# Kernel tuning notes

Measured on AMD Instinct MI355X. Metric: run time of the kernel, lower is better.

Reference implementation:

```python
import jax, jax.numpy as jnp
import numpy as np

B, T, D, H, DK, DV = 4, 2048, 1024, 16, 64, 64


def setup_inputs() -> dict:
    key = jax.random.key(0)
    ks = jax.random.split(key, 7)
    # Glorot-uniform-ish init for weights
    def glorot(k, shape, fan_in, fan_out):
        lim = jnp.sqrt(6.0 / (fan_in + fan_out))
        return jax.random.uniform(k, shape, jnp.float32, -lim, lim)
    Q = jax.random.normal(ks[0], (B, T, D), jnp.float32)
    K = jax.random.normal(ks[1], (B, T, D), jnp.float32)
    V = jax.random.normal(ks[2], (B, T, D), jnp.float32)
    WQ = glorot(ks[3], (H, D, DK), D, DK)
    WK = glorot(ks[4], (H, D, DK), D, DK)
    WV = glorot(ks[5], (H, D, DV), D, DV)
    WO = glorot(ks[6], (H * DV, D), H * DV, D)
    # additive causal mask: 1 where attention is blocked (j > i)
    mask = jnp.triu(jnp.ones((T, T), jnp.float32), k=1)[None, None]  # [1,1,T,T]
    return {"Q": Q, "K": K, "V": V, "WQ": WQ, "WK": WK, "WV": WV, "WO": WO, "mask": mask}


def reference(Q, K, V, WQ, WK, WV, WO, mask):
    Qh = jnp.einsum('btd,hdk->bhtk', Q, WQ)
    Kh = jnp.einsum('btd,hdk->bhtk', K, WK)
    Vh = jnp.einsum('btd,hdv->bhtv', V, WV)
    dk = jnp.asarray(Qh.shape[-1], Qh.dtype)
    logits = jnp.einsum('bhtk,bhsk->bhts', Qh, Kh) / jnp.sqrt(dk)
    logits = logits + mask * (-1e9)
    attn = jax.nn.softmax(logits, axis=-1)
    Ah = jnp.einsum('bhts,bhsv->bhtv', attn, Vh)          # [B,H,T,DV]
    A = jnp.transpose(Ah, (0, 2, 1, 3)).reshape(Ah.shape[0], Ah.shape[2], -1)  # [B,T,H*DV]
    return A @ WO
```

## Files before the change

### kernel.cpp

```cpp
#include <hip/hip_runtime.h>
#include <hip/hip_bf16.h>

#define B_ 4
#define T_ 2048
#define D_ 1024
#define H_ 16

typedef __attribute__((ext_vector_type(8))) short bf16x8;
typedef __attribute__((ext_vector_type(4))) float f32x4;
typedef __attribute__((ext_vector_type(4))) unsigned short u16x4;

__device__ __forceinline__ unsigned short f2bf(float x) {
  union { float f; unsigned u; } v; v.f = x;
  unsigned r = v.u + 0x7fffu + ((v.u >> 16) & 1u);
  return (unsigned short)(r >> 16);
}

__device__ __forceinline__ unsigned pack_bf2(float a, float b) {
  __hip_bfloat162 h = __float22bfloat162_rn(float2{a, b});
  union { __hip_bfloat162 h; unsigned u; } cv; cv.h = h; return cv.u;
}

__device__ __forceinline__ void gload_lds16(const void* g, void* l) {
  __builtin_amdgcn_global_load_lds(
      (const __attribute__((address_space(1))) unsigned int*)g,
      (__attribute__((address_space(3))) unsigned int*)l, 16, 0, 0);
}

#define MFMA16(a, b, c) __builtin_amdgcn_mfma_f32_16x16x32_bf16((a), (b), (c), 0, 0, 0)

__global__ __launch_bounds__(256) void conv3(
    const float4* __restrict__ Q, const float4* __restrict__ K,
    const float4* __restrict__ V, u16x4* __restrict__ Qb,
    u16x4* __restrict__ Kb, u16x4* __restrict__ Vb) {
  const int seg = blockIdx.x >> 10;
  const int sb  = blockIdx.x & 1023;
  const float4* s = (seg == 0) ? Q : (seg == 1) ? K : V;
  u16x4* d       = (seg == 0) ? Qb : (seg == 1) ? Kb : Vb;
  int i = sb * 256 + threadIdx.x;
#pragma unroll
  for (int it = 0; it < 8; ++it, i += 262144) {
    float4 v = s[i];
    u16x4 o;
    o[0] = f2bf(v.x); o[1] = f2bf(v.y); o[2] = f2bf(v.z); o[3] = f2bf(v.w);
    d[i] = o;
  }
}

__global__ __launch_bounds__(256) void trans4(
    const float* __restrict__ WQ, const float* __restrict__ WK,
    const float* __restrict__ WV, const float* __restrict__ WO,
    unsigned short* __restrict__ WqT, unsigned short* __restrict__ WkT,
    unsigned short* __restrict__ WvT, unsigned short* __restrict__ WOt) {
  __shared__ float tile[64][65];
  const int seg = blockIdx.x >> 8;
  const int sub = blockIdx.x & 255;
  const float* src = (seg == 0) ? WQ : (seg == 1) ? WK : (seg == 2) ? WV : WO;
  unsigned short* dst = (seg == 0) ? WqT : (seg == 1) ? WkT : (seg == 2) ? WvT : WOt;
  const int DK = (seg == 3) ? 1024 : 64;
  int h, dt, ktile;
  if (seg == 3) { h = 0; dt = sub >> 4; ktile = sub & 15; }
  else          { h = sub >> 4; dt = sub & 15; ktile = 0; }
  const int d0 = dt * 64, k0 = ktile * 64;
  const int tx = threadIdx.x & 63, ty = threadIdx.x >> 6;
  const float* s = src + (size_t)h * 1024 * DK;
#pragma unroll
  for (int i = 0; i < 16; ++i) {
    int row = i * 4 + ty;
    tile[row][tx] = s[(size_t)(d0 + row) * DK + k0 + tx];
  }
  __syncthreads();
  unsigned short* dd = dst + (size_t)h * DK * 1024;
#pragma unroll
  for (int i = 0; i < 16; ++i) {
    int kk = i * 4 + ty;
    dd[(size_t)(k0 + kk) * 1024 + d0 + tx] = f2bf(tile[tx][kk]);
  }
}

__device__ __forceinline__ void gemm_body(
    const unsigned short* __restrict__ A, const unsigned short* __restrict__ Bt,
    void* __restrict__ C, int bid, int nTilesN, int mode, float scale) {
  __shared__ unsigned short As[128 * 64];
  __shared__ unsigned short Bs[128 * 64];
  const int bm = bid / nTilesN, bn = bid % nTilesN;
  const int m0 = bm * 128, n0 = bn * 128;
  const int tid = threadIdx.x;
  const int wave = tid >> 6, lane = tid & 63;
  const int wr = wave >> 1, wc = wave & 1;

  f32x4 acc[4][4];
#pragma unroll
  for (int m = 0; m < 4; ++m)
#pragma unroll
    for (int n = 0; n < 4; ++n) acc[m][n] = 0.f;

  const int soff = wave * 1024 + lane * 16;
  const char* Afr = (const char*)As + (wr * 64 + (lane & 15)) * 128 + (lane >> 4) * 16;
  const char* Bfr = (const char*)Bs + (wc * 64 + (lane & 15)) * 128 + (lane >> 4) * 16;

  for (int kt = 0; kt < 16; ++kt) {
    __syncthreads();
#pragma unroll
    for (int i = 0; i < 4; ++i) {
      int o2 = i * 4096 + soff;
      int row = o2 >> 7, colb = o2 & 127;
      gload_lds16((const char*)(A + (size_t)(m0 + row) * 1024 + kt * 64) + colb,
                  (char*)As + i * 4096 + wave * 1024);
      gload_lds16((const char*)(Bt + (size_t)(n0 + row) * 1024 + kt * 64) + colb,
                  (char*)Bs + i * 4096 + wave * 1024);
    }
    __syncthreads();
#pragma unroll
    for (int kk = 0; kk < 2; ++kk) {
      bf16x8 af[4], bf[4];
#pragma unroll
      for (int m = 0; m < 4; ++m) af[m] = *(const bf16x8*)(Afr + m * 2048 + kk * 64);
#pragma unroll
      for (int n = 0; n < 4; ++n) bf[n] = *(const bf16x8*)(Bfr + n * 2048 + kk * 64);
#pragma unroll
      for (int m = 0; m < 4; ++m)
#pragma unroll
        for (int n = 0; n < 4; ++n) acc[m][n] = MFMA16(af[m], bf[n], acc[m][n]);
    }
  }

  const int rbase = m0 + wr * 64 + ((lane >> 4) << 2);
  const int cbase = n0 + wc * 64 + (lane & 15);
#pragma unroll
  for (int m = 0; m < 4; ++m)
#pragma unroll
    for (int n = 0; n < 4; ++n)
#pragma unroll
      for (int r = 0; r < 4; ++r) {
        int row = rbase + m * 16 + r;
        int col = cbase + n * 16;
        float v = acc[m][n][r] * scale;
        if (mode == 0) {
          ((float*)C)[(size_t)row * 1024 + col] = v;
        } else if (mode == 1) {
          int b = row >> 11, t = row & 2047, h = col >> 6, k = col & 63;
          ((unsigned short*)C)[(((size_t)(b * H_ + h) * T_) + t) * 64 + k] = f2bf(v);
        } else {
          int h = row >> 6, vv = row & 63, b = col >> 11, t = col & 2047;
          ((unsigned short*)C)[(((size_t)(b * H_ + h) * 64) + vv) * T_ + t] = f2bf(v);
        }
      }
}

__global__ __launch_bounds__(256) void gemm_proj3(
    const unsigned short* __restrict__ Qbf, const unsigned short* __restrict__ WqT,
    unsigned short* __restrict__ Qh,
    const unsigned short* __restrict__ Kbf, const unsigned short* __restrict__ WkT,
    unsigned short* __restrict__ Kh,
    const unsigned short* __restrict__ WvT, const unsigned short* __restrict__ Vbf,
    unsigned short* __restrict__ VhT, float qscale) {
  const int bid = blockIdx.x;
  const int wid = (bid & 7) * 192 + (bid >> 3);
  const int seg = wid / 512, sub = wid % 512;
  const unsigned short* A  = (seg == 0) ? Qbf : (seg == 1) ? Kbf : WvT;
  const unsigned short* Bt = (seg == 0) ? WqT : (seg == 1) ? WkT : Vbf;
  void* C = (seg == 0) ? (void*)Qh : (seg == 1) ? (void*)Kh : (void*)VhT;
  gemm_body(A, Bt, C, sub, (seg == 2) ? 64 : 8, (seg == 2) ? 2 : 1,
            (seg == 0) ? qscale : 1.0f);
}

__global__ __launch_bounds__(256) void gemm_out(
    const unsigned short* __restrict__ A, const unsigned short* __restrict__ Bt,
    float* __restrict__ C) {
  const int bid = blockIdx.x;
  const int wid = (bid & 7) * 64 + (bid >> 3);
  gemm_body(A, Bt, C, wid, 8, 0, 1.0f);
}

__global__ __launch_bounds__(256) void attn_fwd(
    const unsigned short* __restrict__ Qh, const unsigned short* __restrict__ Kh,
    const unsigned short* __restrict__ VhT, unsigned short* __restrict__ Abuf) {
  __shared__ unsigned short Ks[2][64 * 64];
  __shared__ unsigned short Vs[2][64 * 64];
  __shared__ unsigned short Ps[4][16 * 64];

  const int bid = blockIdx.x;
  const int wid = ((bid & 7) << 7) | (bid >> 3);
  const int p  = wid & 15;
  const int bh = wid >> 4;
  const int b = bh >> 4, h = bh & 15;
  const int tid = threadIdx.x;
  const int wave = tid >> 6, lane = tid & 63;
  const int lq = lane & 15;
  const int hi = lane >> 4;
  const int nkt = 32 - p;

  int q0[2];
  q0[0] = (31 - p) * 64 + wave * 16;
  q0[1] = p * 64 + wave * 16;

  const char* Kbase = (const char*)(Kh + (size_t)bh * T_ * 64);
  const char* Vbase = (const char*)(VhT + (size_t)bh * 64 * T_);

  int srow[2], scol[2], sdst[2];
#pragma unroll
  for (int i = 0; i < 2; ++i) {
    int o = i * 4096 + wave * 1024 + lane * 16;
    srow[i] = o >> 7;
    scol[i] = (o & 127) ^ ((srow[i] & 7) << 4);
    sdst[i] = i * 4096 + wave * 1024;
  }

  bf16x8 qf[2][2];
#pragma unroll
  for (int j = 0; j < 2; ++j) {
    const unsigned short* qp = Qh + ((size_t)bh * T_ + q0[j] + lq) * 64 + hi * 8;
    qf[j][0] = *(const bf16x8*)qp;
    qf[j][1] = *(const bf16x8*)(qp + 32);
  }

  f32x4 o[2][4];
#pragma unroll
  for (int j = 0; j < 2; ++j)
#pragma unroll
    for (int n = 0; n < 4; ++n) o[j][n] = 0.f;
  float m_run[2] = {-1e30f, -1e30f}, l_run[2] = {0.f, 0.f};

  const int pswz = (lq & 7) << 4;
  char* pw = (char*)&Ps[wave][0] + lq * 128;

  auto stage = [&](int buf, int kt) {
#pragma unroll
    for (int i = 0; i < 2; ++i) {
      gload_lds16(Kbase + (size_t)(kt * 64 + srow[i]) * 128 + scol[i],
                  (char*)Ks[buf] + sdst[i]);
      gload_lds16(Vbase + (size_t)srow[i] * (T_ * 2) + kt * 128 + scol[i],
                  (char*)Vs[buf] + sdst[i]);
    }
  };

  stage(0, 0);
  asm volatile("s_waitcnt vmcnt(0)" ::: "memory");
  __builtin_amdgcn_s_barrier();

  int cur = 0;
  for (int kt = 0; kt < nkt; ++kt) {
    const int s0 = kt * 64;
    if (kt + 1 < nkt) stage(cur ^ 1, kt + 1);

    const char* KsB = (const char*)Ks[cur];
    const char* VsB = (const char*)Vs[cur];

#pragma unroll
    for (int j = 0; j < 2; ++j) {
      if (j == 1 && kt > p) continue;

      f32x4 sc[4];
      __builtin_amdgcn_s_setprio(1);
#pragma unroll
      for (int c = 0; c < 4; ++c) {
        int r = c * 16 + lq;
        const char* kb = KsB + r * 128;
        int sw = (r & 7) << 4;
        bf16x8 ka0 = *(const bf16x8*)(kb + ((hi * 16) ^ sw));
        bf16x8 ka1 = *(const bf16x8*)(kb + ((64 + hi * 16) ^ sw));
        f32x4 z = 0.f;
        z = MFMA16(ka0, qf[j][0], z);
        sc[c] = MFMA16(ka1, qf[j][1], z);
      }
      __builtin_amdgcn_s_setprio(0);

      if (s0 + 63 > q0[j]) {
        int qg = q0[j] + lq;
#pragma unroll
        for (int c = 0; c < 4; ++c)
#pragma unroll
          for (int r = 0; r < 4; ++r) {
            int sg = s0 + c * 16 + hi * 4 + r;
            if (sg > qg) sc[c][r] = -1e30f;
          }
      }

      float pmax = sc[0][0];
#pragma unroll
      for (int c = 0; c < 4; ++c)
#pragma unroll
        for (int r = 0; r < 4; ++r) pmax = fmaxf(pmax, sc[c][r]);
      pmax = fmaxf(pmax, __shfl_xor(pmax, 16));
      pmax = fmaxf(pmax, __shfl_xor(pmax, 32));

      if (!__all(pmax - m_run[j] <= 8.f)) {
        float mnew = fmaxf(m_run[j], pmax);
        float corr = __builtin_amdgcn_exp2f(m_run[j] - mnew);
        float cr[4];
#pragma unroll
        for (int r = 0; r < 4; ++r) cr[r] = __shfl(corr, hi * 4 + r);
#pragma unroll
        for (int n = 0; n < 4; ++n)
#pragma unroll
          for (int r = 0; r < 4; ++r) o[j][n][r] *= cr[r];
        l_run[j] *= corr;
        m_run[j] = mnew;
      }

      float psum = 0.f;
#pragma unroll
      for (int c = 0; c < 4; ++c)
#pragma unroll
        for (int r = 0; r < 4; ++r) {
          float pv = __builtin_amdgcn_exp2f(sc[c][r] - m_run[j]);
          sc[c][r] = pv;
          psum += pv;
        }
      psum += __shfl_xor(psum, 16);
      psum += __shfl_xor(psum, 32);
      l_run[j] += psum;

#pragma unroll
      for (int c = 0; c < 4; ++c) {
        uint2 pk;
        pk.x = pack_bf2(sc[c][0], sc[c][1]);
        pk.y = pack_bf2(sc[c][2], sc[c][3]);
        *(uint2*)(pw + ((c * 32 + hi * 8) ^ pswz)) = pk;
      }

      __builtin_amdgcn_s_setprio(1);
#pragma unroll
      for (int ks = 0; ks < 2; ++ks) {
        bf16x8 pa = *(const bf16x8*)(pw + ((ks * 64 + hi * 16) ^ pswz));
#pragma unroll
        for (int n = 0; n < 4; ++n) {
          int rv = n * 16 + lq;
          bf16x8 vb = *(const bf16x8*)(VsB + rv * 128 +
                                       ((ks * 64 + hi * 16) ^ ((rv & 7) << 4)));
          o[j][n] = MFMA16(pa, vb, o[j][n]);
        }
      }
      __builtin_amdgcn_s_setprio(0);
    }

    asm volatile("s_waitcnt vmcnt(0)" ::: "memory");
    __builtin_amdgcn_s_barrier();
    cur ^= 1;
  }

#pragma unroll
  for (int j = 0; j < 2; ++j) {
    float inv[4];
#pragma unroll
    for (int r = 0; r < 4; ++r)
      inv[r] = 1.0f / __shfl(l_run[j], hi * 4 + r);
#pragma unroll
    for (int r = 0; r < 4; ++r) {
      int t = q0[j] + hi * 4 + r;
      size_t base = ((size_t)b * T_ + t) * 1024 + h * 64 + lq;
#pragma unroll
      for (int n = 0; n < 4; ++n)
        Abuf[base + n * 16] = f2bf(o[j][n][r] * inv[r]);
    }
  }
}

extern "C" void kernel_launch(void* const* d_in, const int* in_sizes, int n_in,
                              void* d_out, int out_size, void* d_ws, size_t ws_size,
                              hipStream_t stream) {
  (void)in_sizes; (void)n_in; (void)out_size; (void)ws_size;
  const float* Q  = (const float*)d_in[0];
  const float* K  = (const float*)d_in[1];
  const float* V  = (const float*)d_in[2];
  const float* WQ = (const float*)d_in[3];
  const float* WK = (const float*)d_in[4];
  const float* WV = (const float*)d_in[5];
  const float* WO = (const float*)d_in[6];
  float* out = (float*)d_out;
  char* ws = (char*)d_ws;

  const size_t SZ_ACT = (size_t)8192 * 1024 * 2;
  const size_t SZ_W   = (size_t)1024 * 1024 * 2;
  unsigned short* Qbf = (unsigned short*)(ws);
  unsigned short* Kbf = (unsigned short*)(ws + SZ_ACT);
  unsigned short* Vbf = (unsigned short*)(ws + 2 * SZ_ACT);
  unsigned short* WqT = (unsigned short*)(ws + 3 * SZ_ACT);
  unsigned short* WkT = (unsigned short*)(ws + 3 * SZ_ACT + SZ_W);
  unsigned short* WvT = (unsigned short*)(ws + 3 * SZ_ACT + 2 * SZ_W);
  unsigned short* WOt = (unsigned short*)(ws + 3 * SZ_ACT + 3 * SZ_W);
  unsigned short* Qh  = (unsigned short*)(ws + 3 * SZ_ACT + 4 * SZ_W);
  unsigned short* Kh  = (unsigned short*)(ws + 4 * SZ_ACT + 4 * SZ_W);
  unsigned short* VhT = (unsigned short*)(ws + 5 * SZ_ACT + 4 * SZ_W);
  unsigned short* Abuf = Qbf;

  conv3<<<3072, 256, 0, stream>>>((const float4*)Q, (const float4*)K,
                                  (const float4*)V, (u16x4*)Qbf, (u16x4*)Kbf,
                                  (u16x4*)Vbf);

  trans4<<<1024, 256, 0, stream>>>(WQ, WK, WV, WO, WqT, WkT, WvT, WOt);

  const float qscale = 1.4426950408889634f / 8.0f;
  gemm_proj3<<<1536, 256, 0, stream>>>(Qbf, WqT, Qh, Kbf, WkT, Kh,
                                       WvT, Vbf, VhT, qscale);

  attn_fwd<<<1024, 256, 0, stream>>>(Qh, Kh, VhT, Abuf);

  gemm_out<<<512, 256, 0, stream>>>(Abuf, WOt, out);
}
```

Baseline: 230.4 us.

## Fuse fp32-to-bf16 conversion into projection GEMM loads and keep P in registers

Drops the separate conversion kernel. The projection GEMM now reads fp32 Q/K/V directly, converts to bf16 in registers and stores to LDS, which avoids writing and re-reading bf16 activation copies. In attention, the probability tile no longer round-trips through LDS: it is rearranged into the MFMA A-operand layout with permlane swap instructions, and an occupancy hint is added to launch bounds. The tradeoff is that the GEMM loses the async global-to-LDS path for fp32 operands, so loads go through registers and fetch twice the bytes per tile.

New measurement: 227.1 us, median of 2. No clear change (-1.4%).

```diff
diff --git a/kernel.cpp b/kernel.cpp
--- a/kernel.cpp
+++ b/kernel.cpp
@@ -9,6 +9,7 @@
 typedef __attribute__((ext_vector_type(8))) short bf16x8;
 typedef __attribute__((ext_vector_type(4))) float f32x4;
 typedef __attribute__((ext_vector_type(4))) unsigned short u16x4;
+typedef __attribute__((ext_vector_type(4))) unsigned int u32x4;
 
 __device__ __forceinline__ unsigned short f2bf(float x) {
   union { float f; unsigned u; } v; v.f = x;
@@ -28,24 +29,6 @@
 }
 
 #define MFMA16(a, b, c) __builtin_amdgcn_mfma_f32_16x16x32_bf16((a), (b), (c), 0, 0, 0)
-
-__global__ __launch_bounds__(256) void conv3(
-    const float4* __restrict__ Q, const float4* __restrict__ K,
-    const float4* __restrict__ V, u16x4* __restrict__ Qb,
-    u16x4* __restrict__ Kb, u16x4* __restrict__ Vb) {
-  const int seg = blockIdx.x >> 10;
-  const int sb  = blockIdx.x & 1023;
-  const float4* s = (seg == 0) ? Q : (seg == 1) ? K : V;
-  u16x4* d       = (seg == 0) ? Qb : (seg == 1) ? Kb : Vb;
-  int i = sb * 256 + threadIdx.x;
-#pragma unroll
-  for (int it = 0; it < 8; ++it, i += 262144) {
-    float4 v = s[i];
-    u16x4 o;
-    o[0] = f2bf(v.x); o[1] = f2bf(v.y); o[2] = f2bf(v.z); o[3] = f2bf(v.w);
-    d[i] = o;
-  }
-}
 
 __global__ __launch_bounds__(256) void trans4(
     const float* __restrict__ WQ, const float* __restrict__ WK,
@@ -78,9 +61,10 @@
   }
 }
 
+template <bool AF32, bool BF32, int CMODE>
 __device__ __forceinline__ void gemm_body(
-    const unsigned short* __restrict__ A, const unsigned short* __restrict__ Bt,
-    void* __restrict__ C, int bid, int nTilesN, int mode, float scale) {
+    const void* __restrict__ Ap, const void* __restrict__ Btp,
+    void* __restrict__ C, int bid, int nTilesN, float scale) {
   __shared__ unsigned short As[128 * 64];
   __shared__ unsigned short Bs[128 * 64];
   const int bm = bid / nTilesN, bn = bid % nTilesN;
@@ -105,10 +89,32 @@
     for (int i = 0; i < 4; ++i) {
       int o2 = i * 4096 + soff;
       int row = o2 >> 7, colb = o2 & 127;
-      gload_lds16((const char*)(A + (size_t)(m0 + row) * 1024 + kt * 64) + colb,
-                  (char*)As + i * 4096 + wave * 1024);
-      gload_lds16((const char*)(Bt + (size_t)(n0 + row) * 1024 + kt * 64) + colb,
-                  (char*)Bs + i * 4096 + wave * 1024);
+      if constexpr (AF32) {
+        const float* src = (const float*)Ap + (size_t)(m0 + row) * 1024 + kt * 64 + (colb >> 1);
+        float4 f0 = *(const float4*)src;
+        float4 f1 = *(const float4*)(src + 4);
+        u32x4 w;
+        w[0] = pack_bf2(f0.x, f0.y); w[1] = pack_bf2(f0.z, f0.w);
+        w[2] = pack_bf2(f1.x, f1.y); w[3] = pack_bf2(f1.z, f1.w);
+        *(u32x4*)((char*)As + o2) = w;
+      } else {
+        gload_lds16((const char*)((const unsigned short*)Ap +
+                        (size_t)(m0 + row) * 1024 + kt * 64) + colb,
+                    (char*)As + i * 4096 + wave * 1024);
+      }
+      if constexpr (BF32) {
+        const float* src = (const float*)Btp + (size_t)(n0 + row) * 1024 + kt * 64 + (colb >> 1);
+        float4 f0 = *(const float4*)src;
+        float4 f1 = *(const float4*)(src + 4);
+        u32x4 w;
+        w[0] = pack_bf2(f0.x, f0.y); w[1] = pack_bf2(f0.z, f0.w);
+        w[2] = pack_bf2(f1.x, f1.y); w[3] = pack_bf2(f1.z, f1.w);
+        *(u32x4*)((char*)Bs + o2) = w;
+      } else {
+        gload_lds16((const char*)((const unsigned short*)Btp +
+                        (size_t)(n0 + row) * 1024 + kt * 64) + colb,
+                    (char*)Bs + i * 4096 + wave * 1024);
+      }
     }
     __syncthreads();
 #pragma unroll
@@ -136,9 +142,9 @@
         int row = rbase + m * 16 + r;
         int col = cbase + n * 16;
         float v = acc[m][n][r] * scale;
-        if (mode == 0) {
+        if constexpr (CMODE == 0) {
           ((float*)C)[(size_t)row * 1024 + col] = v;
-        } else if (mode == 1) {
+        } else if constexpr (CMODE == 1) {
           int b = row >> 11, t = row & 2047, h = col >> 6, k = col & 63;
           ((unsigned short*)C)[(((size_t)(b * H_ + h) * T_) + t) * 64 + k] = f2bf(v);
         } else {
@@ -149,20 +155,18 @@
 }
 
 __global__ __launch_bounds__(256) void gemm_proj3(
-    const unsigned short* __restrict__ Qbf, const unsigned short* __restrict__ WqT,
+    const float* __restrict__ Q, const unsigned short* __restrict__ WqT,
     unsigned short* __restrict__ Qh,
-    const unsigned short* __restrict__ Kbf, const unsigned short* __restrict__ WkT,
+    const float* __restrict__ K, const unsigned short* __restrict__ WkT,
     unsigned short* __restrict__ Kh,
-    const unsigned short* __restrict__ WvT, const unsigned short* __restrict__ Vbf,
+    const unsigned short* __restrict__ WvT, const float* __restrict__ V,
     unsigned short* __restrict__ VhT, float qscale) {
   const int bid = blockIdx.x;
   const int wid = (bid & 7) * 192 + (bid >> 3);
   const int seg = wid / 512, sub = wid % 512;
-  const unsigned short* A  = (seg == 0) ? Qbf : (seg == 1) ? Kbf : WvT;
-  const unsigned short* Bt = (seg == 0) ? WqT : (seg == 1) ? WkT : Vbf;
-  void* C = (seg == 0) ? (void*)Qh : (seg == 1) ? (void*)Kh : (void*)VhT;
-  gemm_body(A, Bt, C, sub, (seg == 2) ? 64 : 8, (seg == 2) ? 2 : 1,
-            (seg == 0) ? qscale : 1.0f);
+  if (seg == 0)      gemm_body<true,  false, 1>(Q,   WqT, Qh,  sub, 8,  qscale);
+  else if (seg == 1) gemm_body<true,  false, 1>(K,   WkT, Kh,  sub, 8,  1.0f);
+  else               gemm_body<false, true,  2>(WvT, V,   VhT, sub, 64, 1.0f);
 }
 
 __global__ __launch_bounds__(256) void gemm_out(
@@ -170,15 +174,14 @@
     float* __restrict__ C) {
   const int bid = blockIdx.x;
   const int wid = (bid & 7) * 64 + (bid >> 3);
-  gemm_body(A, Bt, C, wid, 8, 0, 1.0f);
-}
-
-__global__ __launch_bounds__(256) void attn_fwd(
+  gemm_body<false, false, 0>(A, Bt, C, wid, 8, 1.0f);
+}
+
+__global__ __launch_bounds__(256, 5) void attn_fwd(
     const unsigned short* __restrict__ Qh, const unsigned short* __restrict__ Kh,
     const unsigned short* __restrict__ VhT, unsigned short* __restrict__ Abuf) {
   __shared__ unsigned short Ks[2][64 * 64];
   __shared__ unsigned short Vs[2][64 * 64];
-  __shared__ unsigned short Ps[4][16 * 64];
 
   const int bid = blockIdx.x;
   const int wid = ((bid & 7) << 7) | (bid >> 3);
@@ -222,9 +225,6 @@
     for (int n = 0; n < 4; ++n) o[j][n] = 0.f;
   float m_run[2] = {-1e30f, -1e30f}, l_run[2] = {0.f, 0.f};
 
-  const int pswz = (lq & 7) << 4;
-  char* pw = (char*)&Ps[wave][0] + lq * 128;
-
   auto stage = [&](int buf, int kt) {
 #pragma unroll
     for (int i = 0; i < 2; ++i) {
@@ -312,18 +312,25 @@
       psum += __shfl_xor(psum, 32);
       l_run[j] += psum;
 
+      unsigned pk[4][2];
 #pragma unroll
       for (int c = 0; c < 4; ++c) {
-        uint2 pk;
-        pk.x = pack_bf2(sc[c][0], sc[c][1]);
-        pk.y = pack_bf2(sc[c][2], sc[c][3]);
-        *(uint2*)(pw + ((c * 32 + hi * 8) ^ pswz)) = pk;
+        pk[c][0] = pack_bf2(sc[c][0], sc[c][1]);
+        pk[c][1] = pack_bf2(sc[c][2], sc[c][3]);
       }
 
       __builtin_amdgcn_s_setprio(1);
 #pragma unroll
       for (int ks = 0; ks < 2; ++ks) {
-        bf16x8 pa = *(const bf16x8*)(pw + ((ks * 64 + hi * 16) ^ pswz));
+        unsigned a0 = pk[2 * ks][0], b0 = pk[2 * ks + 1][0];
+        unsigned a1 = pk[2 * ks][1], b1 = pk[2 * ks + 1][1];
+        asm("v_permlane32_swap_b32 %0, %1" : "+v"(a0), "+v"(b0));
+        asm("v_permlane16_swap_b32 %0, %1" : "+v"(a0), "+v"(b0));
+        asm("v_permlane32_swap_b32 %0, %1" : "+v"(a1), "+v"(b1));
+        asm("v_permlane16_swap_b32 %0, %1" : "+v"(a1), "+v"(b1));
+        u32x4 pau;
+        pau[0] = a0; pau[1] = a1; pau[2] = b0; pau[3] = b1;
+        bf16x8 pa = __builtin_bit_cast(bf16x8, pau);
 #pragma unroll
         for (int n = 0; n < 4; ++n) {
           int rv = n * 16 + lq;
@@ -373,27 +380,20 @@
 
   const size_t SZ_ACT = (size_t)8192 * 1024 * 2;
   const size_t SZ_W   = (size_t)1024 * 1024 * 2;
-  unsigned short* Qbf = (unsigned short*)(ws);
-  unsigned short* Kbf = (unsigned short*)(ws + SZ_ACT);
-  unsigned short* Vbf = (unsigned short*)(ws + 2 * SZ_ACT);
-  unsigned short* WqT = (unsigned short*)(ws + 3 * SZ_ACT);
-  unsigned short* WkT = (unsigned short*)(ws + 3 * SZ_ACT + SZ_W);
-  unsigned short* WvT = (unsigned short*)(ws + 3 * SZ_ACT + 2 * SZ_W);
-  unsigned short* WOt = (unsigned short*)(ws + 3 * SZ_ACT + 3 * SZ_W);
-  unsigned short* Qh  = (unsigned short*)(ws + 3 * SZ_ACT + 4 * SZ_W);
-  unsigned short* Kh  = (unsigned short*)(ws + 4 * SZ_ACT + 4 * SZ_W);
-  unsigned short* VhT = (unsigned short*)(ws + 5 * SZ_ACT + 4 * SZ_W);
-  unsigned short* Abuf = Qbf;
-
-  conv3<<<3072, 256, 0, stream>>>((const float4*)Q, (const float4*)K,
-                                  (const float4*)V, (u16x4*)Qbf, (u16x4*)Kbf,
-                                  (u16x4*)Vbf);
+  unsigned short* WqT = (unsigned short*)(ws);
+  unsigned short* WkT = (unsigned short*)(ws + SZ_W);
+  unsigned short* WvT = (unsigned short*)(ws + 2 * SZ_W);
+  unsigned short* WOt = (unsigned short*)(ws + 3 * SZ_W);
+  unsigned short* Qh  = (unsigned short*)(ws + 4 * SZ_W);
+  unsigned short* Kh  = (unsigned short*)(ws + 4 * SZ_W + SZ_ACT);
+  unsigned short* VhT = (unsigned short*)(ws + 4 * SZ_W + 2 * SZ_ACT);
+  unsigned short* Abuf = (unsigned short*)(ws + 4 * SZ_W + 3 * SZ_ACT);
 
   trans4<<<1024, 256, 0, stream>>>(WQ, WK, WV, WO, WqT, WkT, WvT, WOt);
 
   const float qscale = 1.4426950408889634f / 8.0f;
-  gemm_proj3<<<1536, 256, 0, stream>>>(Qbf, WqT, Qh, Kbf, WkT, Kh,
-                                       WvT, Vbf, VhT, qscale);
+  gemm_proj3<<<1536, 256, 0, stream>>>(Q, WqT, Qh, K, WkT, Kh,
+                                       WvT, V, VhT, qscale);
 
   attn_fwd<<<1024, 256, 0, stream>>>(Qh, Kh, VhT, Abuf);
 
```

## Merge prep kernels, template GEMM epilogue, use permlane swaps for P operand

Applied to the files above, without the earlier changes.

Merges the input cast and weight transpose kernels into one launch. The GEMM epilogue mode becomes a template parameter so the store branch is resolved at compile time. In attention, the probability tile is rearranged into the MFMA A-operand layout with v_permlane32/16 swaps in registers instead of a round trip through LDS, which removes the Ps buffer and adds a launch_bounds occupancy hint of 5. The permlane lane mapping must match the old LDS swizzle exactly, or the results will be wrong.

New measurement: 221.5 us. -3.9%, faster.

```diff
diff --git a/kernel.cpp b/kernel.cpp
--- a/kernel.cpp
+++ b/kernel.cpp
@@ -9,6 +9,7 @@
 typedef __attribute__((ext_vector_type(8))) short bf16x8;
 typedef __attribute__((ext_vector_type(4))) float f32x4;
 typedef __attribute__((ext_vector_type(4))) unsigned short u16x4;
+typedef __attribute__((ext_vector_type(4))) unsigned int u32x4;
 
 __device__ __forceinline__ unsigned short f2bf(float x) {
   union { float f; unsigned u; } v; v.f = x;
@@ -29,60 +30,62 @@
 
 #define MFMA16(a, b, c) __builtin_amdgcn_mfma_f32_16x16x32_bf16((a), (b), (c), 0, 0, 0)
 
-__global__ __launch_bounds__(256) void conv3(
+__global__ __launch_bounds__(256) void prep(
     const float4* __restrict__ Q, const float4* __restrict__ K,
     const float4* __restrict__ V, u16x4* __restrict__ Qb,
-    u16x4* __restrict__ Kb, u16x4* __restrict__ Vb) {
-  const int seg = blockIdx.x >> 10;
-  const int sb  = blockIdx.x & 1023;
-  const float4* s = (seg == 0) ? Q : (seg == 1) ? K : V;
-  u16x4* d       = (seg == 0) ? Qb : (seg == 1) ? Kb : Vb;
-  int i = sb * 256 + threadIdx.x;
-#pragma unroll
-  for (int it = 0; it < 8; ++it, i += 262144) {
-    float4 v = s[i];
-    u16x4 o;
-    o[0] = f2bf(v.x); o[1] = f2bf(v.y); o[2] = f2bf(v.z); o[3] = f2bf(v.w);
-    d[i] = o;
-  }
-}
-
-__global__ __launch_bounds__(256) void trans4(
+    u16x4* __restrict__ Kb, u16x4* __restrict__ Vb,
     const float* __restrict__ WQ, const float* __restrict__ WK,
     const float* __restrict__ WV, const float* __restrict__ WO,
     unsigned short* __restrict__ WqT, unsigned short* __restrict__ WkT,
     unsigned short* __restrict__ WvT, unsigned short* __restrict__ WOt) {
   __shared__ float tile[64][65];
-  const int seg = blockIdx.x >> 8;
-  const int sub = blockIdx.x & 255;
-  const float* src = (seg == 0) ? WQ : (seg == 1) ? WK : (seg == 2) ? WV : WO;
-  unsigned short* dst = (seg == 0) ? WqT : (seg == 1) ? WkT : (seg == 2) ? WvT : WOt;
-  const int DK = (seg == 3) ? 1024 : 64;
-  int h, dt, ktile;
-  if (seg == 3) { h = 0; dt = sub >> 4; ktile = sub & 15; }
-  else          { h = sub >> 4; dt = sub & 15; ktile = 0; }
-  const int d0 = dt * 64, k0 = ktile * 64;
-  const int tx = threadIdx.x & 63, ty = threadIdx.x >> 6;
-  const float* s = src + (size_t)h * 1024 * DK;
-#pragma unroll
-  for (int i = 0; i < 16; ++i) {
-    int row = i * 4 + ty;
-    tile[row][tx] = s[(size_t)(d0 + row) * DK + k0 + tx];
-  }
-  __syncthreads();
-  unsigned short* dd = dst + (size_t)h * DK * 1024;
-#pragma unroll
-  for (int i = 0; i < 16; ++i) {
-    int kk = i * 4 + ty;
-    dd[(size_t)(k0 + kk) * 1024 + d0 + tx] = f2bf(tile[tx][kk]);
-  }
-}
-
+  const int bidx = blockIdx.x;
+  if (bidx < 3072) {
+    const int seg = bidx >> 10;
+    const int sb  = bidx & 1023;
+    const float4* s = (seg == 0) ? Q : (seg == 1) ? K : V;
+    u16x4* d       = (seg == 0) ? Qb : (seg == 1) ? Kb : Vb;
+    int i = sb * 256 + threadIdx.x;
+#pragma unroll
+    for (int it = 0; it < 8; ++it, i += 262144) {
+      float4 v = s[i];
+      u16x4 o;
+      o[0] = f2bf(v.x); o[1] = f2bf(v.y); o[2] = f2bf(v.z); o[3] = f2bf(v.w);
+      d[i] = o;
+    }
+  } else {
+    const int sub4 = bidx - 3072;
+    const int seg = sub4 >> 8;
+    const int sub = sub4 & 255;
+    const float* src = (seg == 0) ? WQ : (seg == 1) ? WK : (seg == 2) ? WV : WO;
+    unsigned short* dst = (seg == 0) ? WqT : (seg == 1) ? WkT : (seg == 2) ? WvT : WOt;
+    const int DK = (seg == 3) ? 1024 : 64;
+    int h, dt, ktile;
+    if (seg == 3) { h = 0; dt = sub >> 4; ktile = sub & 15; }
+    else          { h = sub >> 4; dt = sub & 15; ktile = 0; }
+    const int d0 = dt * 64, k0 = ktile * 64;
+    const int tx = threadIdx.x & 63, ty = threadIdx.x >> 6;
+    const float* s = src + (size_t)h * 1024 * DK;
+#pragma unroll
+    for (int i = 0; i < 16; ++i) {
+      int row = i * 4 + ty;
+      tile[row][tx] = s[(size_t)(d0 + row) * DK + k0 + tx];
+    }
+    __syncthreads();
+    unsigned short* dd = dst + (size_t)h * DK * 1024;
+#pragma unroll
+    for (int i = 0; i < 16; ++i) {
+      int kk = i * 4 + ty;
+      dd[(size_t)(k0 + kk) * 1024 + d0 + tx] = f2bf(tile[tx][kk]);
+    }
+  }
+}
+
+template <int CMODE>
 __device__ __forceinline__ void gemm_body(
+    unsigned short* __restrict__ As, unsigned short* __restrict__ Bs,
     const unsigned short* __restrict__ A, const unsigned short* __restrict__ Bt,
-    void* __restrict__ C, int bid, int nTilesN, int mode, float scale) {
-  __shared__ unsigned short As[128 * 64];
-  __shared__ unsigned short Bs[128 * 64];
+    void* __restrict__ C, int bid, int nTilesN, float scale) {
   const int bm = bid / nTilesN, bn = bid % nTilesN;
   const int m0 = bm * 128, n0 = bn * 128;
   const int tid = threadIdx.x;
@@ -136,9 +139,9 @@
         int row = rbase + m * 16 + r;
         int col = cbase + n * 16;
         float v = acc[m][n][r] * scale;
-        if (mode == 0) {
+        if constexpr (CMODE == 0) {
           ((float*)C)[(size_t)row * 1024 + col] = v;
-        } else if (mode == 1) {
+        } else if constexpr (CMODE == 1) {
           int b = row >> 11, t = row & 2047, h = col >> 6, k = col & 63;
           ((unsigned short*)C)[(((size_t)(b * H_ + h) * T_) + t) * 64 + k] = f2bf(v);
         } else {
@@ -155,30 +158,31 @@
     unsigned short* __restrict__ Kh,
     const unsigned short* __restrict__ WvT, const unsigned short* __restrict__ Vbf,
     unsigned short* __restrict__ VhT, float qscale) {
+  __shared__ unsigned short As[128 * 64];
+  __shared__ unsigned short Bs[128 * 64];
   const int bid = blockIdx.x;
   const int wid = (bid & 7) * 192 + (bid >> 3);
   const int seg = wid / 512, sub = wid % 512;
-  const unsigned short* A  = (seg == 0) ? Qbf : (seg == 1) ? Kbf : WvT;
-  const unsigned short* Bt = (seg == 0) ? WqT : (seg == 1) ? WkT : Vbf;
-  void* C = (seg == 0) ? (void*)Qh : (seg == 1) ? (void*)Kh : (void*)VhT;
-  gemm_body(A, Bt, C, sub, (seg == 2) ? 64 : 8, (seg == 2) ? 2 : 1,
-            (seg == 0) ? qscale : 1.0f);
+  if (seg == 0)      gemm_body<1>(As, Bs, Qbf, WqT, Qh,  sub, 8,  qscale);
+  else if (seg == 1) gemm_body<1>(As, Bs, Kbf, WkT, Kh,  sub, 8,  1.0f);
+  else               gemm_body<2>(As, Bs, WvT, Vbf, VhT, sub, 64, 1.0f);
 }
 
 __global__ __launch_bounds__(256) void gemm_out(
     const unsigned short* __restrict__ A, const unsigned short* __restrict__ Bt,
     float* __restrict__ C) {
+  __shared__ unsigned short As[128 * 64];
+  __shared__ unsigned short Bs[128 * 64];
   const int bid = blockIdx.x;
   const int wid = (bid & 7) * 64 + (bid >> 3);
-  gemm_body(A, Bt, C, wid, 8, 0, 1.0f);
-}
-
-__global__ __launch_bounds__(256) void attn_fwd(
+  gemm_body<0>(As, Bs, A, Bt, C, wid, 8, 1.0f);
+}
+
+__global__ __launch_bounds__(256, 5) void attn_fwd(
     const unsigned short* __restrict__ Qh, const unsigned short* __restrict__ Kh,
     const unsigned short* __restrict__ VhT, unsigned short* __restrict__ Abuf) {
   __shared__ unsigned short Ks[2][64 * 64];
   __shared__ unsigned short Vs[2][64 * 64];
-  __shared__ unsigned short Ps[4][16 * 64];
 
   const int bid = blockIdx.x;
   const int wid = ((bid & 7) << 7) | (bid >> 3);
@@ -222,9 +226,6 @@
     for (int n = 0; n < 4; ++n) o[j][n] = 0.f;
   float m_run[2] = {-1e30f, -1e30f}, l_run[2] = {0.f, 0.f};
 
-  const int pswz = (lq & 7) << 4;
-  char* pw = (char*)&Ps[wave][0] + lq * 128;
-
   auto stage = [&](int buf, int kt) {
 #pragma unroll
     for (int i = 0; i < 2; ++i) {
@@ -312,18 +313,25 @@
       psum += __shfl_xor(psum, 32);
       l_run[j] += psum;
 
+      unsigned pk[4][2];
 #pragma unroll
       for (int c = 0; c < 4; ++c) {
-        uint2 pk;
-        pk.x = pack_bf2(sc[c][0], sc[c][1]);
-        pk.y = pack_bf2(sc[c][2], sc[c][3]);
-        *(uint2*)(pw + ((c * 32 + hi * 8) ^ pswz)) = pk;
+        pk[c][0] = pack_bf2(sc[c][0], sc[c][1]);
+        pk[c][1] = pack_bf2(sc[c][2], sc[c][3]);
       }
 
       __builtin_amdgcn_s_setprio(1);
 #pragma unroll
       for (int ks = 0; ks < 2; ++ks) {
-        bf16x8 pa = *(const bf16x8*)(pw + ((ks * 64 + hi * 16) ^ pswz));
+        unsigned a0 = pk[2 * ks][0], b0 = pk[2 * ks + 1][0];
+        unsigned a1 = pk[2 * ks][1], b1 = pk[2 * ks + 1][1];
+        asm("v_permlane32_swap_b32 %0, %1" : "+v"(a0), "+v"(b0));
+        asm("v_permlane16_swap_b32 %0, %1" : "+v"(a0), "+v"(b0));
+        asm("v_permlane32_swap_b32 %0, %1" : "+v"(a1), "+v"(b1));
+        asm("v_permlane16_swap_b32 %0, %1" : "+v"(a1), "+v"(b1));
+        u32x4 pau;
+        pau[0] = a0; pau[1] = a1; pau[2] = b0; pau[3] = b1;
+        bf16x8 pa = __builtin_bit_cast(bf16x8, pau);
 #pragma unroll
         for (int n = 0; n < 4; ++n) {
           int rv = n * 16 + lq;
@@ -385,11 +393,10 @@
   unsigned short* VhT = (unsigned short*)(ws + 5 * SZ_ACT + 4 * SZ_W);
   unsigned short* Abuf = Qbf;
 
-  conv3<<<3072, 256, 0, stream>>>((const float4*)Q, (const float4*)K,
-                                  (const float4*)V, (u16x4*)Qbf, (u16x4*)Kbf,
-                                  (u16x4*)Vbf);
-
-  trans4<<<1024, 256, 0, stream>>>(WQ, WK, WV, WO, WqT, WkT, WvT, WOt);
+  prep<<<4096, 256, 0, stream>>>((const float4*)Q, (const float4*)K,
+                                 (const float4*)V, (u16x4*)Qbf, (u16x4*)Kbf,
+                                 (u16x4*)Vbf, WQ, WK, WV, WO,
+                                 WqT, WkT, WvT, WOt);
 
   const float qscale = 1.4426950408889634f / 8.0f;
   gemm_proj3<<<1536, 256, 0, stream>>>(Qbf, WqT, Qh, Kbf, WkT, Kh,
```
